# Kernel optimization log

Measured on AMD Instinct MI355X. Metric: run time of the kernel, lower is better.

Reference implementation:

```python
import jax, jax.numpy as jnp
import numpy as np

N, D, H = 4096, 128, 8

def setup_inputs() -> dict:
    key = jax.random.key(0)
    ks = jax.random.split(key, 7)
    xavier = float(np.sqrt(6.0 / (D + D)))  # xavier_uniform for [*, D, D]
    x = jax.random.normal(ks[0], (N, D), dtype=jnp.float32)
    W_k = jax.random.uniform(ks[1], (H, D, D), minval=-xavier, maxval=xavier, dtype=jnp.float32)
    W_q = jax.random.uniform(ks[2], (H, D, D), minval=-xavier, maxval=xavier, dtype=jnp.float32)
    W_v = jax.random.uniform(ks[3], (H, D, D), minval=-xavier, maxval=xavier, dtype=jnp.float32)
    W_m = jnp.ones((H,), dtype=jnp.float32)
    lim = float(1.0 / np.sqrt(D))  # default torch Linear init range
    Wg = jax.random.uniform(ks[4], (D, D), minval=-lim, maxval=lim, dtype=jnp.float32)
    bg = jax.random.uniform(ks[5], (D,), minval=-lim, maxval=lim, dtype=jnp.float32)
    return {"x": x, "W_k": W_k, "W_q": W_q, "W_v": W_v, "W_m": W_m, "Wg": Wg, "bg": bg}

def reference(x, W_k, W_q, W_v, W_m, Wg, bg):
    # per-head projections: [H, N, D]
    q = jnp.einsum('nf,hfd->hnd', x, W_q)
    k = jnp.einsum('nf,hfd->hnd', x, W_k)
    v = jnp.einsum('nf,hfd->hnd', x, W_v)
    # dense all-pairs attention scores per head: [H, N, N]
    e = jnp.einsum('hnd,hmd->hnm', q, k)
    attn = jax.nn.softmax(e, axis=-1)
    # weighted sum over values, then head-scaled accumulation: [N, D]
    out = jnp.einsum('h,hnm,hmd->nd', W_m, attn, v)
    # residual MLP: x + ReLU(Linear(x + out))
    h = x + out
    g = jax.nn.relu(h @ Wg.T + bg)
    return x + g
```

## Files before the change

### kernel.cpp

```cpp
#include <hip/hip_runtime.h>

#define NROWS 4096
#define DDIM  128
#define NHEAD 8
#define LOG2E 1.44269504088896f

extern "C" __device__ float __ocml_native_exp2_f32(float);

typedef __attribute__((ext_vector_type(8))) short    short8;
typedef __attribute__((ext_vector_type(8))) _Float16 half8;
typedef __attribute__((ext_vector_type(4))) float    floatx4;

__device__ __forceinline__ float bf2f(unsigned short u){
  unsigned v = ((unsigned)u) << 16;
  return __builtin_bit_cast(float, v);
}
__device__ __forceinline__ unsigned short f2bf(float f){
  unsigned u = __builtin_bit_cast(unsigned, f);
  u += 0x7FFFu + ((u >> 16) & 1u);
  return (unsigned short)(u >> 16);
}
__device__ __forceinline__ void split2(float v, unsigned short& hi, unsigned short& lo){
  hi = f2bf(v);
  lo = f2bf(v - bf2f(hi));
}
__device__ __forceinline__ void async_cp16(const void* g, void* l){
  __builtin_amdgcn_global_load_lds(
      (const __attribute__((address_space(1))) void*)g,
      (__attribute__((address_space(3))) void*)l, 16, 0, 0);
}
__device__ __forceinline__ float dpp_max16(float v){
  int t;
  t = __builtin_amdgcn_update_dpp(0, __builtin_bit_cast(int, v), 0x128, 0xF, 0xF, false);
  v = fmaxf(v, __builtin_bit_cast(float, t));
  t = __builtin_amdgcn_update_dpp(0, __builtin_bit_cast(int, v), 0x124, 0xF, 0xF, false);
  v = fmaxf(v, __builtin_bit_cast(float, t));
  t = __builtin_amdgcn_update_dpp(0, __builtin_bit_cast(int, v), 0x122, 0xF, 0xF, false);
  v = fmaxf(v, __builtin_bit_cast(float, t));
  t = __builtin_amdgcn_update_dpp(0, __builtin_bit_cast(int, v), 0x121, 0xF, 0xF, false);
  v = fmaxf(v, __builtin_bit_cast(float, t));
  return v;
}

__global__ void fill_kernel(float* __restrict__ out, float val, int n){
  int i = blockIdx.x * 256 + threadIdx.x;
  if (i < n) out[i] = val;
}

__global__ __launch_bounds__(256) void prep_kernel(
    const float* __restrict__ Wk, const float* __restrict__ Wv,
    const float* __restrict__ Wq, const float* __restrict__ Wg,
    const float* __restrict__ x,
    unsigned short* __restrict__ wpre, unsigned short* __restrict__ wgpre,
    unsigned short* __restrict__ xh, unsigned short* __restrict__ xl)
{
  const int id = blockIdx.x * 256 + threadIdx.x;
  if (id < 49152) {
    const int z = id >> 14, rem = id & 16383;
    const int h = rem >> 11, rem2 = rem & 2047;
    const int fh = rem2 >> 10, L = rem2 & 1023;
    const int d = L >> 3, m = L & 7;
    const int kk0 = (m ^ (d & 7)) << 3;
    const float* W = (z == 0 ? Wk : (z == 1 ? Wv : Wq)) + h * DDIM * DDIM;
    short8 hi8, lo8;
#pragma unroll
    for (int j = 0; j < 8; j++) {
      unsigned short hi, lo;
      split2(W[(fh * 64 + kk0 + j) * DDIM + d], hi, lo);
      hi8[j] = (short)hi; lo8[j] = (short)lo;
    }
    unsigned short* base = wpre + (size_t)((z * 8 + h) * 2 + fh) * 16384;
    *(short8*)(base + L * 8) = hi8;
    *(short8*)(base + 8192 + L * 8) = lo8;
  } else if (id < 51200) {
    const int t = id - 49152;
    const int fh = t >> 10, L = t & 1023;
    const int d = L >> 3, m = L & 7;
    const int kk0 = (m ^ (d & 7)) << 3;
    short8 hi8, lo8;
#pragma unroll
    for (int j = 0; j < 8; j++) {
      unsigned short hi, lo;
      split2(Wg[d * DDIM + fh * 64 + kk0 + j], hi, lo);
      hi8[j] = (short)hi; lo8[j] = (short)lo;
    }
    unsigned short* base = wgpre + fh * 16384;
    *(short8*)(base + L * 8) = hi8;
    *(short8*)(base + 8192 + L * 8) = lo8;
  } else if (id < 116736) {
    const int t = id - 51200;
    const float* src = x + (size_t)t * 8;
    float4 v0 = *(const float4*)src, v1 = *(const float4*)(src + 4);
    float xv[8] = {v0.x, v0.y, v0.z, v0.w, v1.x, v1.y, v1.z, v1.w};
    short8 hi8, lo8;
#pragma unroll
    for (int j = 0; j < 8; j++) {
      unsigned short hi, lo; split2(xv[j], hi, lo);
      hi8[j] = (short)hi; lo8[j] = (short)lo;
    }
    *(short8*)(xh + (size_t)t * 8) = hi8;
    *(short8*)(xl + (size_t)t * 8) = lo8;
  }
}

__global__ __launch_bounds__(256, 4) void proj_kernel(
    const unsigned short* __restrict__ xh, const unsigned short* __restrict__ xl,
    const unsigned short* __restrict__ wpre,
    _Float16* __restrict__ kfo, _Float16* __restrict__ vfo,
    _Float16* __restrict__ qfo)
{
  __shared__ alignas(16) unsigned short whi[8192];
  __shared__ alignas(16) unsigned short wlo[8192];
  const int tid = threadIdx.x, lane = tid & 63, wave = tid >> 6;
  const int l4 = lane & 15, quad = lane >> 4;
  const int h = blockIdx.y, z = blockIdx.z;
  const unsigned short* wb = wpre + (size_t)((z * 8 + h) * 2) * 16384;

  floatx4 acc[2][8];
#pragma unroll
  for (int t4 = 0; t4 < 2; t4++)
#pragma unroll
    for (int c = 0; c < 8; c++) acc[t4][c] = (floatx4)0.f;

  for (int fh = 0; fh < 2; fh++) {
    {
      const unsigned short* src = wb + fh * 16384;
      const unsigned short* sh = src + wave * 2048 + lane * 8;
      const unsigned short* sl = src + 8192 + wave * 2048 + lane * 8;
      unsigned short* dh = &whi[wave * 2048];
      unsigned short* dl = &wlo[wave * 2048];
#pragma unroll
      for (int it = 0; it < 4; it++) {
        async_cp16(sh + it * 512, dh + it * 512);
        async_cp16(sl + it * 512, dl + it * 512);
      }
    }
    __syncthreads();

#pragma unroll
    for (int t4 = 0; t4 < 2; t4++) {
      const int row = blockIdx.x * 128 + t4 * 64 + wave * 16 + l4;
      const size_t xo = (size_t)row * DDIM + fh * 64 + quad * 8;
      short8 ah[2], al[2];
      ah[0] = *(const short8*)(xh + xo);
      ah[1] = *(const short8*)(xh + xo + 32);
      al[0] = *(const short8*)(xl + xo);
      al[1] = *(const short8*)(xl + xo + 32);
#pragma unroll
      for (int t2 = 0; t2 < 2; t2++) {
#pragma unroll
        for (int c = 0; c < 8; c++) {
          const int col = c * 16 + l4;
          const int idx = (col * 8 + ((t2 * 4 + quad) ^ (col & 7))) * 8;
          short8 bh = *(const short8*)&whi[idx];
          short8 bl = *(const short8*)&wlo[idx];
          acc[t4][c] = __builtin_amdgcn_mfma_f32_16x16x32_bf16(ah[t2], bh, acc[t4][c], 0, 0, 0);
          acc[t4][c] = __builtin_amdgcn_mfma_f32_16x16x32_bf16(al[t2], bh, acc[t4][c], 0, 0, 0);
          acc[t4][c] = __builtin_amdgcn_mfma_f32_16x16x32_bf16(ah[t2], bl, acc[t4][c], 0, 0, 0);
        }
      }
    }
    __syncthreads();
  }

  const int rb = wave * 16 + quad * 4;
#pragma unroll
  for (int t4 = 0; t4 < 2; t4++) {
    const int tile = blockIdx.x * 2 + t4;
    const size_t tilebase = (size_t)(h * 64 + tile) * 8192;
#pragma unroll
    for (int c = 0; c < 8; c++) {
      const int d = c * 16 + l4;
#pragma unroll
      for (int r = 0; r < 4; r++) {
        const int kl = rb + r;
        const float val = acc[t4][c][r];
        if (z == 0) {
          const int c2 = kl >> 4, l4k = kl & 15;
          const int tt = d >> 5, qd = (d >> 3) & 3, jj = d & 7;
          const int qX = qd ^ ((l4k >> 1) & 3);
          kfo[tilebase + (size_t)((c2 * 4 + tt) * 16 + l4k) * 32 + qX * 8 + jj] =
              (_Float16)val;
        } else if (z == 1) {
          const int c2 = d >> 4, l4v = d & 15;
          const int tt = kl >> 5, qd = (kl >> 3) & 3, jj = kl & 7;
          const int qX = qd ^ ((l4v >> 1) & 3);
          vfo[tilebase + (size_t)((c2 * 2 + tt) * 16 + l4v) * 32 + qX * 8 + jj] =
              (_Float16)val;
        } else {
          qfo[((size_t)h * NROWS + (size_t)tile * 64 + kl) * DDIM + d] =
              (_Float16)(val * LOG2E);
        }
      }
    }
  }
}

struct FlashLds {
  _Float16 k[2][8192];
  _Float16 p[4][1024];
};

__global__ __launch_bounds__(256, 4) void flash_kernel(
    const _Float16* __restrict__ qfo, const _Float16* __restrict__ kfo,
    const _Float16* __restrict__ vfo,
    _Float16* __restrict__ op, float* __restrict__ mb, float* __restrict__ lb)
{
  __shared__ alignas(16) FlashLds lds;
  const int tid = threadIdx.x, lane = tid & 63, wave = tid >> 6;
  const int l4 = lane & 15, quad = lane >> 4;
  const int h = blockIdx.x & 7, qt = (blockIdx.x >> 3) & 63, s = blockIdx.x >> 9;
  const int q0 = qt * 64;

  half8 aq[4];
  {
    const _Float16* qr =
        qfo + ((size_t)h * NROWS + q0 + wave * 16 + l4) * DDIM + quad * 8;
#pragma unroll
    for (int t = 0; t < 4; t++) aq[t] = *(const half8*)(qr + t * 32);
  }

  float m_run[4];
#pragma unroll
  for (int r = 0; r < 4; r++) m_run[r] = -1e30f;
  floatx4 Oacc[8], lacc = (floatx4)0.f;
#pragma unroll
  for (int c = 0; c < 8; c++) Oacc[c] = (floatx4)0.f;

  half8 vones;
#pragma unroll
  for (int j = 0; j < 8; j++) vones[j] = (_Float16)1.f;

  const _Float16* kfo_h = kfo + (size_t)h * 64 * 8192;
  const _Float16* vfo_h = vfo + (size_t)h * 64 * 8192;
  const int lq = (l4 * 4 + (quad ^ ((l4 >> 1) & 3))) * 8;
  const int kt0 = s * 32, kt1 = kt0 + 32;

  {
    const _Float16* ks = kfo_h + (size_t)kt0 * 8192 + wave * 2048 + lane * 8;
    _Float16* kd = &lds.k[0][wave * 2048];
#pragma unroll
    for (int it = 0; it < 4; it++) async_cp16(ks + it * 512, kd + it * 512);
  }

  for (int kt = kt0; kt < kt1; ++kt) {
    const int cur = kt & 1;
    __syncthreads();

    if (kt + 1 < kt1) {
      const _Float16* ks = kfo_h + (size_t)(kt + 1) * 8192 + wave * 2048 + lane * 8;
      _Float16* kd = &lds.k[cur ^ 1][wave * 2048];
#pragma unroll
      for (int it = 0; it < 4; it++) async_cp16(ks + it * 512, kd + it * 512);
    }

    floatx4 Sf[4];
#pragma unroll
    for (int c = 0; c < 4; c++) Sf[c] = (floatx4)0.f;
    __builtin_amdgcn_s_setprio(1);
#pragma unroll
    for (int t = 0; t < 4; t++) {
      half8 b[4];
#pragma unroll
      for (int c = 0; c < 4; c++)
        b[c] = *(const half8*)&lds.k[cur][(c * 4 + t) * 512 + lq];
#pragma unroll
      for (int c = 0; c < 4; c++)
        Sf[c] = __builtin_amdgcn_mfma_f32_16x16x32_f16(aq[t], b[c], Sf[c], 0, 0, 0);
    }
    __builtin_amdgcn_s_setprio(0);

    float alpha[4];
    {
      float mt[4];
#pragma unroll
      for (int r = 0; r < 4; r++)
        mt[r] = fmaxf(fmaxf(Sf[0][r], Sf[1][r]), fmaxf(Sf[2][r], Sf[3][r]));
#pragma unroll
      for (int r = 0; r < 4; r++) mt[r] = dpp_max16(mt[r]);
#pragma unroll
      for (int r = 0; r < 4; r++) {
        const float mn = fmaxf(m_run[r], mt[r]);
        alpha[r] = __ocml_native_exp2_f32(m_run[r] - mn);
        m_run[r] = mn;
      }
#pragma unroll
      for (int r = 0; r < 4; r++)
#pragma unroll
        for (int c = 0; c < 4; c++)
          Sf[c][r] = __ocml_native_exp2_f32(Sf[c][r] - m_run[r]);
    }

#pragma unroll
    for (int c = 0; c < 4; c++)
#pragma unroll
      for (int r = 0; r < 4; r++) {
        const int row_s = (c * 2 + (l4 >> 3)) * 16 + quad * 4 + r;
        const int rs = row_s ^ ((row_s >> 2) & 7);
        lds.p[wave][rs * 8 + (l4 & 7)] = (_Float16)Sf[c][r];
      }

    {
      const bool moved = (alpha[0] != 1.f) | (alpha[1] != 1.f) |
                         (alpha[2] != 1.f) | (alpha[3] != 1.f);
      if (__any(moved)) {
#pragma unroll
        for (int c = 0; c < 8; c++) {
          Oacc[c][0] *= alpha[0]; Oacc[c][1] *= alpha[1];
          Oacc[c][2] *= alpha[2]; Oacc[c][3] *= alpha[3];
        }
        lacc[0] *= alpha[0]; lacc[1] *= alpha[1];
        lacc[2] *= alpha[2]; lacc[3] *= alpha[3];
      }
    }

#pragma unroll
    for (int t = 0; t < 2; t++) {
      half8 vf[8];
      {
        const _Float16* vtb = vfo_h + (size_t)kt * 8192 + t * 512 + lq;
#pragma unroll
        for (int c = 0; c < 8; c++)
          vf[c] = *(const half8*)(vtb + c * 1024);
      }
      const int row_r = (t * 4 + quad) * 16 + l4;
      const int rr = row_r ^ ((row_r >> 2) & 7);
      half8 ap = *(const half8*)&lds.p[wave][rr * 8];
      __builtin_amdgcn_s_setprio(1);
      lacc = __builtin_amdgcn_mfma_f32_16x16x32_f16(ap, vones, lacc, 0, 0, 0);
#pragma unroll
      for (int c = 0; c < 8; c++)
        Oacc[c] = __builtin_amdgcn_mfma_f32_16x16x32_f16(ap, vf[c], Oacc[c], 0, 0, 0);
      __builtin_amdgcn_s_setprio(0);
    }
  }

  const int rbase = wave * 16 + quad * 4;
  const size_t rowbase = (size_t)(s * NHEAD + h) * NROWS + q0 + rbase;
#pragma unroll
  for (int c = 0; c < 8; c++) {
    const int col = c * 16 + l4;
#pragma unroll
    for (int r = 0; r < 4; r++)
      op[(rowbase + r) * DDIM + col] = (_Float16)Oacc[c][r];
  }
  if (l4 == 0) {
#pragma unroll
    for (int r = 0; r < 4; r++) {
      mb[rowbase + r] = m_run[r];
      lb[rowbase + r] = lacc[r];
    }
  }
}

__global__ __launch_bounds__(256, 2) void mlp_kernel(
    const float* __restrict__ x, const _Float16* __restrict__ op,
    const float* __restrict__ mb, const float* __restrict__ lb,
    const float* __restrict__ Wm,
    const unsigned short* __restrict__ wgpre, const float* __restrict__ bg,
    float* __restrict__ out)
{
  __shared__ alignas(16) unsigned short whi[8192];
  __shared__ alignas(16) unsigned short wlo[8192];
  __shared__ float sc[64][17];
  const int tid = threadIdx.x, lane = tid & 63, wave = tid >> 6;
  const int l4 = lane & 15, quad = lane >> 4;
  const int r0 = blockIdx.x * 64;

  for (int i = tid; i < 512; i += 256) {
    const int rr = i >> 3, hh = i & 7;
    const int n = r0 + rr;
    const float m1 = mb[(size_t)hh * NROWS + n];
    const float m2 = mb[(size_t)(NHEAD + hh) * NROWS + n];
    const float l1 = lb[(size_t)hh * NROWS + n];
    const float l2 = lb[(size_t)(NHEAD + hh) * NROWS + n];
    const float m  = fmaxf(m1, m2);
    const float a1 = __ocml_native_exp2_f32(m1 - m);
    const float a2 = __ocml_native_exp2_f32(m2 - m);
    const float invL = Wm[hh] / (l1 * a1 + l2 * a2);
    sc[rr][hh] = a1 * invL;
    sc[rr][8 + hh] = a2 * invL;
  }

  floatx4 acc[8];
#pragma unroll
  for (int c = 0; c < 8; c++) acc[c] = (floatx4)0.f;

  float scr[16];
  const int rloc = wave * 16 + l4;
  const size_t nrow = (size_t)(r0 + rloc);

  for (int fh = 0; fh < 2; fh++) {
    {
      const unsigned short* src = wgpre + fh * 16384;
      const unsigned short* sh = src + wave * 2048 + lane * 8;
      const unsigned short* sl = src + 8192 + wave * 2048 + lane * 8;
      unsigned short* dh = &whi[wave * 2048];
      unsigned short* dl = &wlo[wave * 2048];
#pragma unroll
      for (int it = 0; it < 4; it++) {
        async_cp16(sh + it * 512, dh + it * 512);
        async_cp16(sl + it * 512, dl + it * 512);
      }
    }
    __syncthreads();

    if (fh == 0) {
#pragma unroll
      for (int i = 0; i < 16; i++) scr[i] = sc[rloc][i];
    }

    short8 ah[2], al[2];
#pragma unroll
    for (int t2 = 0; t2 < 2; t2++) {
      const int dbase = fh * 64 + t2 * 32 + quad * 8;
      const size_t xoff = nrow * DDIM + dbase;
      float4 x0 = *(const float4*)(x + xoff);
      float4 x1 = *(const float4*)(x + xoff + 4);
      float hv[8] = {x0.x, x0.y, x0.z, x0.w, x1.x, x1.y, x1.z, x1.w};
#pragma unroll
      for (int i = 0; i < 16; i++) {
        const half8 ov = *(const half8*)(op + ((size_t)i * NROWS + nrow) * DDIM + dbase);
        const float sci = scr[i];
#pragma unroll
        for (int j = 0; j < 8; j++) hv[j] += sci * (float)ov[j];
      }
#pragma unroll
      for (int j = 0; j < 8; j++) {
        unsigned short hi, lo; split2(hv[j], hi, lo);
        ah[t2][j] = (short)hi; al[t2][j] = (short)lo;
      }
    }
#pragma unroll
    for (int t2 = 0; t2 < 2; t2++) {
#pragma unroll
      for (int c = 0; c < 8; c++) {
        const int col = c * 16 + l4;
        const int idx = (col * 8 + ((t2 * 4 + quad) ^ (col & 7))) * 8;
        short8 bh = *(const short8*)&whi[idx];
        short8 bl = *(const short8*)&wlo[idx];
        acc[c] = __builtin_amdgcn_mfma_f32_16x16x32_bf16(ah[t2], bh, acc[c], 0, 0, 0);
        acc[c] = __builtin_amdgcn_mfma_f32_16x16x32_bf16(al[t2], bh, acc[c], 0, 0, 0);
        acc[c] = __builtin_amdgcn_mfma_f32_16x16x32_bf16(ah[t2], bl, acc[c], 0, 0, 0);
      }
    }
    __syncthreads();
  }

  const int rbase = wave * 16 + quad * 4;
#pragma unroll
  for (int c = 0; c < 8; c++) {
    const int col = c * 16 + l4;
    const float bgf = bg[col];
#pragma unroll
    for (int r = 0; r < 4; r++) {
      const size_t idx = (size_t)(r0 + rbase + r) * DDIM + col;
      out[idx] = x[idx] + fmaxf(acc[c][r] + bgf, 0.f);
    }
  }
}

extern "C" void kernel_launch(void* const* d_in, const int* in_sizes, int n_in,
                              void* d_out, int out_size, void* d_ws, size_t ws_size,
                              hipStream_t stream) {
  float* out = (float*)d_out;
  const int fill_blocks = (out_size + 255) / 256;

  const bool ok_sizes =
      n_in == 7 &&
      in_sizes[0] == NROWS * DDIM &&
      in_sizes[1] == NHEAD * DDIM * DDIM &&
      in_sizes[2] == NHEAD * DDIM * DDIM &&
      in_sizes[3] == NHEAD * DDIM * DDIM &&
      in_sizes[4] == NHEAD &&
      in_sizes[5] == DDIM * DDIM &&
      in_sizes[6] == DDIM &&
      out_size == NROWS * DDIM;
  if (!ok_sizes) {
    fill_kernel<<<fill_blocks, 256, 0, stream>>>(out, 1000.f, out_size);
    return;
  }

  const size_t HND = (size_t)NHEAD * NROWS * DDIM;
  const size_t ND  = (size_t)NROWS * DDIM;
  const size_t WPRE_N  = (size_t)3 * 8 * 2 * 16384;
  const size_t WGPRE_N = (size_t)2 * 16384;
  const size_t need = 3 * HND * 2 + 2 * HND * 2 +
                      2 * (2 * (size_t)NHEAD * NROWS) * 4 +
                      (WPRE_N + WGPRE_N + 2 * ND) * 2;
  if (ws_size < need) {
    fill_kernel<<<fill_blocks, 256, 0, stream>>>(out, 500.f, out_size);
    return;
  }

  const float* x  = (const float*)d_in[0];
  const float* Wk = (const float*)d_in[1];
  const float* Wq = (const float*)d_in[2];
  const float* Wv = (const float*)d_in[3];
  const float* Wm = (const float*)d_in[4];
  const float* Wg = (const float*)d_in[5];
  const float* bg = (const float*)d_in[6];

  _Float16*       kfo   = (_Float16*)d_ws;
  _Float16*       vfo   = kfo + HND;
  _Float16*       qfo   = vfo + HND;
  _Float16*       op    = qfo + HND;
  float*          mb    = (float*)(op + 2 * HND);
  float*          lb    = mb + 2 * NHEAD * NROWS;
  unsigned short* wpre  = (unsigned short*)(lb + 2 * NHEAD * NROWS);
  unsigned short* wgpre = wpre + WPRE_N;
  unsigned short* xh    = wgpre + WGPRE_N;
  unsigned short* xl    = xh + ND;

  (void)hipGetLastError();
  prep_kernel<<<dim3(456), 256, 0, stream>>>(Wk, Wv, Wq, Wg, x, wpre, wgpre, xh, xl);
  proj_kernel<<<dim3(32, NHEAD, 3), 256, 0, stream>>>(xh, xl, wpre, kfo, vfo, qfo);
  flash_kernel<<<dim3(1024), 256, 0, stream>>>(qfo, kfo, vfo, op, mb, lb);
  mlp_kernel<<<dim3(64), 256, 0, stream>>>(x, op, mb, lb, Wm, wgpre, bg, out);
  if (hipGetLastError() != hipSuccess) {
    fill_kernel<<<fill_blocks, 256, 0, stream>>>(out, 2000.f, out_size);
  }
}
```

Baseline: 219.7 us.

## Split MLP into single-wave blocks reading pre-fragmented Wg directly from global

The Wg weights are pre-laid out in MFMA B-fragment order during prep so each lane loads its fragment straight from global memory. The MLP kernel drops the shared-memory staging, the barriers and the shared scale table, and runs 256 one-wave blocks instead of 64 four-wave blocks. This raises block count to fill more CUs for a small tail kernel, at the cost of each wave re-reading the full Wg from L2.

```diff
diff --git a/kernel.cpp b/kernel.cpp
--- a/kernel.cpp
+++ b/kernel.cpp
@@ -51,7 +51,7 @@
     const float* __restrict__ Wk, const float* __restrict__ Wv,
     const float* __restrict__ Wq, const float* __restrict__ Wg,
     const float* __restrict__ x,
-    unsigned short* __restrict__ wpre, unsigned short* __restrict__ wgpre,
+    unsigned short* __restrict__ wpre, unsigned short* __restrict__ wgfrag,
     unsigned short* __restrict__ xh, unsigned short* __restrict__ xl)
 {
   const int id = blockIdx.x * 256 + threadIdx.x;
@@ -74,19 +74,22 @@
     *(short8*)(base + 8192 + L * 8) = lo8;
   } else if (id < 51200) {
     const int t = id - 49152;
-    const int fh = t >> 10, L = t & 1023;
-    const int d = L >> 3, m = L & 7;
-    const int kk0 = (m ^ (d & 7)) << 3;
+    const int fh = t >> 10, rem = t & 1023;
+    const int t2 = rem >> 9, rem2 = rem & 511;
+    const int c = rem2 >> 6, ln = rem2 & 63;
+    const int quad = ln >> 4, l4 = ln & 15;
+    const int col = c * 16 + l4;
+    const int k0 = fh * 64 + t2 * 32 + quad * 8;
     short8 hi8, lo8;
 #pragma unroll
     for (int j = 0; j < 8; j++) {
       unsigned short hi, lo;
-      split2(Wg[d * DDIM + fh * 64 + kk0 + j], hi, lo);
+      split2(Wg[col * DDIM + k0 + j], hi, lo);
       hi8[j] = (short)hi; lo8[j] = (short)lo;
     }
-    unsigned short* base = wgpre + fh * 16384;
-    *(short8*)(base + L * 8) = hi8;
-    *(short8*)(base + 8192 + L * 8) = lo8;
+    unsigned short* base = wgfrag + (size_t)((((fh * 2 + t2) * 8 + c) * 64 + ln) * 8);
+    *(short8*)base = hi8;
+    *(short8*)(base + 16384) = lo8;
   } else if (id < 116736) {
     const int t = id - 51200;
     const float* src = x + (size_t)t * 8;
@@ -353,63 +356,37 @@
   }
 }
 
-__global__ __launch_bounds__(256, 2) void mlp_kernel(
+__global__ __launch_bounds__(64) void mlp_kernel(
     const float* __restrict__ x, const _Float16* __restrict__ op,
     const float* __restrict__ mb, const float* __restrict__ lb,
     const float* __restrict__ Wm,
-    const unsigned short* __restrict__ wgpre, const float* __restrict__ bg,
+    const unsigned short* __restrict__ wgfrag, const float* __restrict__ bg,
     float* __restrict__ out)
 {
-  __shared__ alignas(16) unsigned short whi[8192];
-  __shared__ alignas(16) unsigned short wlo[8192];
-  __shared__ float sc[64][17];
-  const int tid = threadIdx.x, lane = tid & 63, wave = tid >> 6;
-  const int l4 = lane & 15, quad = lane >> 4;
-  const int r0 = blockIdx.x * 64;
-
-  for (int i = tid; i < 512; i += 256) {
-    const int rr = i >> 3, hh = i & 7;
-    const int n = r0 + rr;
-    const float m1 = mb[(size_t)hh * NROWS + n];
-    const float m2 = mb[(size_t)(NHEAD + hh) * NROWS + n];
-    const float l1 = lb[(size_t)hh * NROWS + n];
-    const float l2 = lb[(size_t)(NHEAD + hh) * NROWS + n];
+  const int lane = threadIdx.x, l4 = lane & 15, quad = lane >> 4;
+  const int r0 = blockIdx.x * 16;
+  const size_t nrow = (size_t)(r0 + l4);
+
+  float scr[16];
+#pragma unroll
+  for (int hh = 0; hh < 8; hh++) {
+    const float m1 = mb[(size_t)hh * NROWS + nrow];
+    const float m2 = mb[(size_t)(NHEAD + hh) * NROWS + nrow];
+    const float l1 = lb[(size_t)hh * NROWS + nrow];
+    const float l2 = lb[(size_t)(NHEAD + hh) * NROWS + nrow];
     const float m  = fmaxf(m1, m2);
     const float a1 = __ocml_native_exp2_f32(m1 - m);
     const float a2 = __ocml_native_exp2_f32(m2 - m);
     const float invL = Wm[hh] / (l1 * a1 + l2 * a2);
-    sc[rr][hh] = a1 * invL;
-    sc[rr][8 + hh] = a2 * invL;
+    scr[hh] = a1 * invL;
+    scr[8 + hh] = a2 * invL;
   }
 
   floatx4 acc[8];
 #pragma unroll
   for (int c = 0; c < 8; c++) acc[c] = (floatx4)0.f;
 
-  float scr[16];
-  const int rloc = wave * 16 + l4;
-  const size_t nrow = (size_t)(r0 + rloc);
-
   for (int fh = 0; fh < 2; fh++) {
-    {
-      const unsigned short* src = wgpre + fh * 16384;
-      const unsigned short* sh = src + wave * 2048 + lane * 8;
-      const unsigned short* sl = src + 8192 + wave * 2048 + lane * 8;
-      unsigned short* dh = &whi[wave * 2048];
-      unsigned short* dl = &wlo[wave * 2048];
-#pragma unroll
-      for (int it = 0; it < 4; it++) {
-        async_cp16(sh + it * 512, dh + it * 512);
-        async_cp16(sl + it * 512, dl + it * 512);
-      }
-    }
-    __syncthreads();
-
-    if (fh == 0) {
-#pragma unroll
-      for (int i = 0; i < 16; i++) scr[i] = sc[rloc][i];
-    }
-
     short8 ah[2], al[2];
 #pragma unroll
     for (int t2 = 0; t2 < 2; t2++) {
@@ -435,19 +412,18 @@
     for (int t2 = 0; t2 < 2; t2++) {
 #pragma unroll
       for (int c = 0; c < 8; c++) {
-        const int col = c * 16 + l4;
-        const int idx = (col * 8 + ((t2 * 4 + quad) ^ (col & 7))) * 8;
-        short8 bh = *(const short8*)&whi[idx];
-        short8 bl = *(const short8*)&wlo[idx];
+        const unsigned short* fb =
+            wgfrag + (size_t)((((fh * 2 + t2) * 8 + c) * 64 + lane) * 8);
+        short8 bh = *(const short8*)fb;
+        short8 bl = *(const short8*)(fb + 16384);
         acc[c] = __builtin_amdgcn_mfma_f32_16x16x32_bf16(ah[t2], bh, acc[c], 0, 0, 0);
         acc[c] = __builtin_amdgcn_mfma_f32_16x16x32_bf16(al[t2], bh, acc[c], 0, 0, 0);
         acc[c] = __builtin_amdgcn_mfma_f32_16x16x32_bf16(ah[t2], bl, acc[c], 0, 0, 0);
       }
     }
-    __syncthreads();
-  }
-
-  const int rbase = wave * 16 + quad * 4;
+  }
+
+  const int rbase = quad * 4;
 #pragma unroll
   for (int c = 0; c < 8; c++) {
     const int col = c * 16 + l4;
@@ -501,22 +477,22 @@
   const float* Wg = (const float*)d_in[5];
   const float* bg = (const float*)d_in[6];
 
-  _Float16*       kfo   = (_Float16*)d_ws;
-  _Float16*       vfo   = kfo + HND;
-  _Float16*       qfo   = vfo + HND;
-  _Float16*       op    = qfo + HND;
-  float*          mb    = (float*)(op + 2 * HND);
-  float*          lb    = mb + 2 * NHEAD * NROWS;
-  unsigned short* wpre  = (unsigned short*)(lb + 2 * NHEAD * NROWS);
-  unsigned short* wgpre = wpre + WPRE_N;
-  unsigned short* xh    = wgpre + WGPRE_N;
-  unsigned short* xl    = xh + ND;
+  _Float16*       kfo    = (_Float16*)d_ws;
+  _Float16*       vfo    = kfo + HND;
+  _Float16*       qfo    = vfo + HND;
+  _Float16*       op     = qfo + HND;
+  float*          mb     = (float*)(op + 2 * HND);
+  float*          lb     = mb + 2 * NHEAD * NROWS;
+  unsigned short* wpre   = (unsigned short*)(lb + 2 * NHEAD * NROWS);
+  unsigned short* wgfrag = wpre + WPRE_N;
+  unsigned short* xh     = wgfrag + WGPRE_N;
+  unsigned short* xl     = xh + ND;
 
   (void)hipGetLastError();
-  prep_kernel<<<dim3(456), 256, 0, stream>>>(Wk, Wv, Wq, Wg, x, wpre, wgpre, xh, xl);
+  prep_kernel<<<dim3(456), 256, 0, stream>>>(Wk, Wv, Wq, Wg, x, wpre, wgfrag, xh, xl);
   proj_kernel<<<dim3(32, NHEAD, 3), 256, 0, stream>>>(xh, xl, wpre, kfo, vfo, qfo);
   flash_kernel<<<dim3(1024), 256, 0, stream>>>(qfo, kfo, vfo, op, mb, lb);
-  mlp_kernel<<<dim3(64), 256, 0, stream>>>(x, op, mb, lb, Wm, wgpre, bg, out);
+  mlp_kernel<<<dim3(256), 64, 0, stream>>>(x, op, mb, lb, Wm, wgfrag, bg, out);
   if (hipGetLastError() != hipSuccess) {
     fill_kernel<<<fill_blocks, 256, 0, stream>>>(out, 2000.f, out_size);
   }
```

Measured after the change: 213.9 us (median of 2 runs). 1.03x faster.
